# Kernel optimization log

Hardware: AMD Instinct MI355X
Metric: run time of the kernel (lower is better)

Reference implementation:

```python
import jax, jax.numpy as jnp
import numpy as np

B, S, H, NH = 4, 2048, 1024, 16
HD = H // NH


def setup_inputs() -> dict:
    key = jax.random.key(0)
    ks = jax.random.split(key, 9)
    s = 1.0 / np.sqrt(H)
    return {
        "x": jax.random.normal(ks[0], (B, S, H), dtype=jnp.float32),
        "wq": jax.random.normal(ks[1], (H, H), dtype=jnp.float32) * s,
        "bq": jax.random.normal(ks[2], (H,), dtype=jnp.float32) * 0.02,
        "wk": jax.random.normal(ks[3], (H, H), dtype=jnp.float32) * s,
        "bk": jax.random.normal(ks[4], (H,), dtype=jnp.float32) * 0.02,
        "wv": jax.random.normal(ks[5], (H, H), dtype=jnp.float32) * s,
        "bv": jax.random.normal(ks[6], (H,), dtype=jnp.float32) * 0.02,
        "wo": jax.random.normal(ks[7], (H, H), dtype=jnp.float32) * s,
        "bo": jax.random.normal(ks[8], (H,), dtype=jnp.float32) * 0.02,
    }


def reference(x, wq, bq, wk, bk, wv, bv, wo, bo):
    b, s, h = x.shape
    def heads(t):  # (b,s,h) -> (b,nh,s,hd)
        return t.reshape(b, s, NH, HD).transpose(0, 2, 1, 3)
    q = heads(x @ wq.T + bq)
    k = heads(x @ wk.T + bk)
    v = heads(x @ wv.T + bv)
    scores = jnp.einsum("bnqd,bnkd->bnqk", q, k) / np.sqrt(HD).astype(np.float32)
    causal = jnp.tril(jnp.ones((s, s), dtype=bool))
    scores = jnp.where(causal[None, None], scores, -jnp.inf)
    probs = jax.nn.softmax(scores, axis=-1)
    out = jnp.einsum("bnqk,bnkd->bnqd", probs, v)
    out = out.transpose(0, 2, 1, 3).reshape(b, s, h)
    return out @ wo.T + bo
```

## Files before the change

### kernel.cpp

```cpp
#include <hip/hip_runtime.h>
#include <hip/hip_bf16.h>

using bf16 = __bf16;
typedef __attribute__((ext_vector_type(4))) bf16 bf16x4;
typedef __attribute__((ext_vector_type(8))) bf16 bf16x8;
typedef __attribute__((ext_vector_type(4))) float f32x4;
typedef __attribute__((ext_vector_type(16))) float f32x16;

constexpr int kB = 4, kS = 2048, kH = 1024, kNH = 16, kHD = 64;
constexpr int kM = kB * kS;

__device__ __forceinline__ float exp2a(float x) {
  float r;
  asm("v_exp_f32 %0, %1" : "=v"(r) : "v"(x));
  return r;
}
__device__ __forceinline__ unsigned cvtpk(float a, float b) {
  unsigned r;
  asm("v_cvt_pk_bf16_f32 %0, %1, %2" : "=v"(r) : "v"(a), "v"(b));
  return r;
}
__device__ __forceinline__ void glds16(const bf16* g, bf16* l) {
  __builtin_amdgcn_global_load_lds(
      (const __attribute__((address_space(1))) unsigned*)g,
      (__attribute__((address_space(3))) unsigned*)l, 16, 0, 0);
}

__global__ __launch_bounds__(256) void cvt_all_kernel(
    const float* __restrict__ x, const float* __restrict__ w0,
    const float* __restrict__ w1, const float* __restrict__ w2,
    const float* __restrict__ w3, bf16* __restrict__ xb,
    bf16* __restrict__ wb) {
  const int blk = blockIdx.x;
  const float* src;
  bf16* dst;
  int rel;
  if (blk < kM) {
    src = x; dst = xb; rel = blk;
  } else {
    const int wi = (blk - kM) >> 10;
    rel = (blk - kM) & 1023;
    src = wi == 0 ? w0 : wi == 1 ? w1 : wi == 2 ? w2 : w3;
    dst = wb + (size_t)wi * kH * kH;
  }
  const size_t i = (size_t)rel * 256 + threadIdx.x;
  const float4 f = ((const float4*)src)[i];
  bf16x4 o;
  o[0] = (bf16)f.x; o[1] = (bf16)f.y; o[2] = (bf16)f.z; o[3] = (bf16)f.w;
  ((bf16x4*)dst)[i] = o;
}

template <int MODE>
__device__ __forceinline__ void mm_body(const bf16* __restrict__ A,
                                        const bf16* __restrict__ W,
                                        const float* __restrict__ bias,
                                        void* __restrict__ Cp, float scale) {
  __shared__ __align__(16) bf16 As[128 * 32];
  __shared__ __align__(16) bf16 Bs[128 * 32];
  const int tid = threadIdx.x;
  const int lane = tid & 63;
  const int wid = tid >> 6;
  const int wr = wid >> 1, wc = wid & 1;
  const int fr = lane & 15, fg = lane >> 4;
  const int bm = blockIdx.x * 128, bn = blockIdx.y * 128;
  const bf16* Ab = A + (size_t)bm * kH;
  const bf16* Wb = W + (size_t)bn * kH;
  const int srow = lane >> 2;
  const int scol = (lane & 3) * 8;
  const int rb0 = wid * 32, rb1 = wid * 32 + 16;

  f32x4 acc[4][4] = {};

  for (int k0 = 0; k0 < kH; k0 += 32) {
    __syncthreads();
    glds16(Ab + (size_t)(rb0 + srow) * kH + k0 + scol, As + rb0 * 32);
    glds16(Ab + (size_t)(rb1 + srow) * kH + k0 + scol, As + rb1 * 32);
    glds16(Wb + (size_t)(rb0 + srow) * kH + k0 + scol, Bs + rb0 * 32);
    glds16(Wb + (size_t)(rb1 + srow) * kH + k0 + scol, Bs + rb1 * 32);
    __syncthreads();

    bf16x8 af[4], bfv[4];
#pragma unroll
    for (int m = 0; m < 4; ++m)
      af[m] = *(const bf16x8*)(As + (wr * 64 + m * 16 + fr) * 32 + fg * 8);
#pragma unroll
    for (int n = 0; n < 4; ++n)
      bfv[n] = *(const bf16x8*)(Bs + (wc * 64 + n * 16 + fr) * 32 + fg * 8);
#pragma unroll
    for (int m = 0; m < 4; ++m)
#pragma unroll
      for (int n = 0; n < 4; ++n)
        acc[m][n] = __builtin_amdgcn_mfma_f32_16x16x32_bf16(af[m], bfv[n],
                                                            acc[m][n], 0, 0, 0);
  }

#pragma unroll
  for (int n = 0; n < 4; ++n) {
    const int nabs = bn + wc * 64 + n * 16 + fr;
    const float bv = bias[nabs];
#pragma unroll
    for (int m = 0; m < 4; ++m) {
      if (MODE == 2) {
        const int tok0 = bm + wr * 64 + m * 16 + fg * 4;
        const int b = tok0 >> 11, s0 = tok0 & (kS - 1);
        const int h = nabs >> 6, d = nabs & 63;
        bf16x4 pv;
#pragma unroll
        for (int reg = 0; reg < 4; ++reg) pv[reg] = (bf16)(acc[m][n][reg] + bv);
        *(bf16x4*)((bf16*)Cp + (((size_t)(b * kNH + h) * kHD + d) * kS + s0)) = pv;
      } else {
#pragma unroll
        for (int reg = 0; reg < 4; ++reg) {
          const int tok = bm + wr * 64 + m * 16 + fg * 4 + reg;
          const float v = (acc[m][n][reg] + bv) * scale;
          if (MODE == 0) {
            ((float*)Cp)[(size_t)tok * kH + nabs] = v;
          } else {
            const int b = tok >> 11, s = tok & (kS - 1);
            const int h = nabs >> 6, d = nabs & 63;
            ((bf16*)Cp)[(((size_t)(b * kNH + h)) * kS + s) * kHD + d] = (bf16)v;
          }
        }
      }
    }
  }
}

__global__ __launch_bounds__(256) void qkv_kernel(
    const bf16* __restrict__ xb, const bf16* __restrict__ wb,
    const float* __restrict__ bq, const float* __restrict__ bk,
    const float* __restrict__ bv, bf16* __restrict__ qh,
    bf16* __restrict__ kh, bf16* __restrict__ vh) {
  const int z = blockIdx.z;
  const bf16* W = wb + (size_t)z * kH * kH;
  if (z == 0) mm_body<1>(xb, W, bq, qh, 0.125f * 1.44269504f);
  else if (z == 1) mm_body<1>(xb, W, bk, kh, 1.f);
  else mm_body<2>(xb, W, bv, vh, 1.f);
}

__global__ __launch_bounds__(256) void oproj_kernel(
    const bf16* __restrict__ ab, const bf16* __restrict__ wob,
    const float* __restrict__ bo, float* __restrict__ out) {
  mm_body<0>(ab, wob, bo, out, 1.f);
}

__global__ __launch_bounds__(256) void attn_kernel(
    const bf16* __restrict__ Qh, const bf16* __restrict__ Kh,
    const bf16* __restrict__ Vt, bf16* __restrict__ Ab) {
  __shared__ __align__(16) bf16 Ks[64 * 64];
  __shared__ __align__(16) bf16 Vs[64 * 64];
  const int tid = threadIdx.x;
  const int lane = tid & 63;
  const int wid = tid >> 6;
  const int l31 = lane & 31;
  const int hi = lane >> 5;
  const int bh = blockIdx.x;
  const int qt = gridDim.y - 1 - blockIdx.y;
  const int b = bh >> 4, h = bh & (kNH - 1);

  const int qfirst = qt * 128 + wid * 32;
  const int qrow = qfirst + l31;

  const bf16* Qg = Qh + (size_t)bh * kS * kHD;
  const bf16* Kg = Kh + (size_t)bh * kS * kHD;
  const bf16* Vg = Vt + (size_t)bh * kHD * kS;

  bf16x8 qf[4];
#pragma unroll
  for (int kb = 0; kb < 4; ++kb)
    qf[kb] = *(const bf16x8*)(Qg + (size_t)qrow * kHD + kb * 16 + hi * 8);

  f32x16 Oa0 = {}, Oa1 = {};
  float lreg = 0.f;

  const int sr = tid >> 2;
  const int sc = tid & 3;
  const int nt64 = qt * 2 + 2;

  for (int kt = 0; kt < nt64; ++kt) {
    const int kt0 = kt * 64;
    const bf16x8 kr0 = *(const bf16x8*)(Kg + (size_t)(kt0 + sr) * kHD + sc * 8);
    const bf16x8 kr1 = *(const bf16x8*)(Kg + (size_t)(kt0 + sr) * kHD + (sc + 4) * 8);
    const bf16x8 vr0 = *(const bf16x8*)(Vg + (size_t)sr * kS + kt0 + sc * 8);
    const bf16x8 vr1 = *(const bf16x8*)(Vg + (size_t)sr * kS + kt0 + (sc + 4) * 8);
    __syncthreads();
    *(bf16x8*)((char*)Ks + sr * 128 + ((sc ^ (sr & 7)) << 4)) = kr0;
    *(bf16x8*)((char*)Ks + sr * 128 + (((sc + 4) ^ (sr & 7)) << 4)) = kr1;
    *(bf16x8*)((char*)Vs + sr * 128 + ((sc ^ (sr & 7)) << 4)) = vr0;
    *(bf16x8*)((char*)Vs + sr * 128 + (((sc + 4) ^ (sr & 7)) << 4)) = vr1;
    __syncthreads();

#pragma unroll
    for (int st = 0; st < 2; ++st) {
      const int kabs = kt0 + st * 32;
      if (kabs > qfirst) continue;
      const bool diag = (kabs == qfirst);

      f32x16 S = {};
      {
        const int row = st * 32 + l31;
        const char* krow = (const char*)Ks + row * 128;
#pragma unroll
        for (int kb = 0; kb < 4; ++kb) {
          const int slot = (kb * 2 + hi) ^ (row & 7);
          const bf16x8 kf = *(const bf16x8*)(krow + slot * 16);
          S = __builtin_amdgcn_mfma_f32_32x32x16_bf16(kf, qf[kb], S, 0, 0, 0);
        }
      }
      bf16x8 vf0[2], vf1[2];
#pragma unroll
      for (int kb2 = 0; kb2 < 2; ++kb2) {
        const int d0 = l31, d1 = 32 + l31;
        const int c = st * 4 + kb2 * 2 + hi;
        vf0[kb2] = *(const bf16x8*)((char*)Vs + d0 * 128 + ((c ^ (d0 & 7)) << 4));
        vf1[kb2] = *(const bf16x8*)((char*)Vs + d1 * 128 + ((c ^ (d1 & 7)) << 4));
      }

      float p[16];
      float ps = 0.f;
      if (diag) {
#pragma unroll
        for (int r = 0; r < 16; ++r) {
          const int key = kabs + (r & 3) + 8 * (r >> 2) + 4 * hi;
          float s2 = S[r] - 8.f;
          if (key > qrow) s2 = -3.0e38f;
          p[r] = exp2a(s2);
          ps += p[r];
        }
      } else {
#pragma unroll
        for (int r = 0; r < 16; ++r) {
          p[r] = exp2a(S[r] - 8.f);
          ps += p[r];
        }
      }
      ps += __shfl_xor(ps, 32, 64);
      lreg += ps;

      bf16x8 pf[2];
#pragma unroll
      for (int kb2 = 0; kb2 < 2; ++kb2) {
        const int o = kb2 * 8;
        unsigned a01 = cvtpk(p[o + 0], p[o + 1]);
        unsigned a45 = cvtpk(p[o + 4], p[o + 5]);
        asm("v_permlane32_swap_b32 %0, %1" : "+v"(a01), "+v"(a45));
        unsigned a23 = cvtpk(p[o + 2], p[o + 3]);
        unsigned a67 = cvtpk(p[o + 6], p[o + 7]);
        asm("v_permlane32_swap_b32 %0, %1" : "+v"(a23), "+v"(a67));
        union { unsigned u[4]; bf16x8 v; } t;
        t.u[0] = a01; t.u[1] = a23; t.u[2] = a45; t.u[3] = a67;
        pf[kb2] = t.v;
      }

#pragma unroll
      for (int kb2 = 0; kb2 < 2; ++kb2) {
        Oa0 = __builtin_amdgcn_mfma_f32_32x32x16_bf16(vf0[kb2], pf[kb2], Oa0, 0, 0, 0);
        Oa1 = __builtin_amdgcn_mfma_f32_32x32x16_bf16(vf1[kb2], pf[kb2], Oa1, 0, 0, 0);
      }
    }
  }

  const float rl = 1.f / lreg;
  bf16* const orow = Ab + ((size_t)b * kS + qrow) * kH + h * 64;
#pragma unroll
  for (int rq = 0; rq < 4; ++rq) {
    bf16x4 o0, o1;
#pragma unroll
    for (int j = 0; j < 4; ++j) {
      o0[j] = (bf16)(Oa0[rq * 4 + j] * rl);
      o1[j] = (bf16)(Oa1[rq * 4 + j] * rl);
    }
    *(bf16x4*)(orow + rq * 8 + hi * 4) = o0;
    *(bf16x4*)(orow + 32 + rq * 8 + hi * 4) = o1;
  }
}

extern "C" void kernel_launch(void* const* d_in, const int* in_sizes, int n_in,
                              void* d_out, int out_size, void* d_ws,
                              size_t ws_size, hipStream_t stream) {
  const float* x = (const float*)d_in[0];
  const float* wq = (const float*)d_in[1];
  const float* bq = (const float*)d_in[2];
  const float* wk = (const float*)d_in[3];
  const float* bk = (const float*)d_in[4];
  const float* wv = (const float*)d_in[5];
  const float* bv = (const float*)d_in[6];
  const float* wo = (const float*)d_in[7];
  const float* bo = (const float*)d_in[8];
  float* out = (float*)d_out;

  const size_t perHead = (size_t)kB * kNH * kS * kHD;
  bf16* xb = (bf16*)d_ws;
  bf16* wb = xb + (size_t)kM * kH;
  bf16* qh = wb + (size_t)4 * kH * kH;
  bf16* kh = qh + perHead;
  bf16* vh = kh + perHead;
  bf16* ab = vh + perHead;

  dim3 blk(256);
  cvt_all_kernel<<<dim3(kM + 4 * 1024), blk, 0, stream>>>(x, wq, wk, wv, wo,
                                                          xb, wb);
  qkv_kernel<<<dim3(kM / 128, kH / 128, 3), blk, 0, stream>>>(
      xb, wb, bq, bk, bv, qh, kh, vh);
  attn_kernel<<<dim3(kB * kNH, kS / 128), blk, 0, stream>>>(qh, kh, vh, ab);
  oproj_kernel<<<dim3(kM / 128, kH / 128), blk, 0, stream>>>(
      ab, wb + (size_t)3 * kH * kH, bo, out);
}
```

Measured before the change: 163.9 us.

## Rewrite QKV GEMM as 256x128 double-buffered 8-wave kernel with XCD remap

Replaces the templated QKV GEMM with a dedicated 512-thread kernel using 256x128 tiles and K=64 steps. It double-buffers LDS through direct global-to-LDS loads with XOR swizzle, interleaves MFMA phases with barriers and priority hints, and remaps block IDs across XCDs for L2 locality. The aim is to hide global load latency and raise data reuse in the dominant GEMM. The attention softmax also drops the constant -8 offset in the exponent, which risks overflow if scores grow large.

```diff
diff --git a/kernel.cpp b/kernel.cpp
--- a/kernel.cpp
+++ b/kernel.cpp
@@ -50,11 +50,133 @@
   ((bf16x4*)dst)[i] = o;
 }
 
-template <int MODE>
-__device__ __forceinline__ void mm_body(const bf16* __restrict__ A,
-                                        const bf16* __restrict__ W,
-                                        const float* __restrict__ bias,
-                                        void* __restrict__ Cp, float scale) {
+constexpr int kNT = 16;
+
+__global__ __launch_bounds__(512) void qkv8_kernel(
+    const bf16* __restrict__ xb, const bf16* __restrict__ wb,
+    const float* __restrict__ bq, const float* __restrict__ bk,
+    const float* __restrict__ bv, bf16* __restrict__ qh,
+    bf16* __restrict__ kh, bf16* __restrict__ vh) {
+  __shared__ __align__(16) bf16 As[2][256 * 64];
+  __shared__ __align__(16) bf16 Bs[2][128 * 64];
+  const int tid = threadIdx.x;
+  const int lane = tid & 63;
+  const int wid = tid >> 6;
+  const int wr = wid & 3;
+  const int wc = wid >> 2;
+  const int fr = lane & 15, fg = lane >> 4;
+
+  const int orig = blockIdx.x;
+  const int wg = (orig & 7) * 96 + (orig >> 3);
+  const int mb = wg & 31;
+  const int nb = wg >> 5;
+  const int bn_g = nb * 128;
+  const int z = bn_g >> 10;
+  const int bn = bn_g & 1023;
+
+  const bf16* Ab = xb + (size_t)mb * 256 * kH;
+  const bf16* Wb = wb + (size_t)z * kH * kH + (size_t)bn * kH;
+
+  const int s_r = lane >> 3;
+  const int s_cs = ((lane & 7) ^ (lane >> 3)) * 8;
+
+  f32x4 acc[4][4] = {};
+  bf16x8 bfr[4];
+
+#define ST(buf, kt)                                                          \
+  do {                                                                       \
+    const int k0_ = (kt) * 64;                                               \
+    _Pragma("unroll") for (int i = 0; i < 4; ++i) {                          \
+      const int rb = wid * 32 + i * 8;                                       \
+      glds16(Ab + (size_t)(rb + s_r) * kH + k0_ + s_cs, As[buf] + rb * 64);  \
+    }                                                                        \
+    _Pragma("unroll") for (int i = 0; i < 2; ++i) {                          \
+      const int rb = wid * 16 + i * 8;                                       \
+      glds16(Wb + (size_t)(rb + s_r) * kH + k0_ + s_cs, Bs[buf] + rb * 64);  \
+    }                                                                        \
+  } while (0)
+
+#define PH(buf, mlo, k2, DOB)                                                \
+  do {                                                                       \
+    const int swzA0 = (((k2)*4 + fg) ^ (fr & 7)) * 8;                        \
+    bf16x8 a0 = *(const bf16x8*)(As[buf] +                                   \
+        (wr * 64 + (mlo)*16 + fr) * 64 + swzA0);                             \
+    bf16x8 a1 = *(const bf16x8*)(As[buf] +                                   \
+        (wr * 64 + ((mlo)+1)*16 + fr) * 64 + swzA0);                         \
+    if (DOB) {                                                               \
+      _Pragma("unroll") for (int n = 0; n < 4; ++n)                          \
+        bfr[n] = *(const bf16x8*)(Bs[buf] +                                  \
+            (wc * 64 + n * 16 + fr) * 64 + swzA0);                           \
+    }                                                                        \
+    __builtin_amdgcn_s_barrier();                                            \
+    asm volatile("s_waitcnt lgkmcnt(0)" ::: "memory");                       \
+    __builtin_amdgcn_sched_barrier(0);                                       \
+    __builtin_amdgcn_s_setprio(1);                                           \
+    _Pragma("unroll") for (int n = 0; n < 4; ++n) {                          \
+      acc[(mlo)][n] = __builtin_amdgcn_mfma_f32_16x16x32_bf16(               \
+          a0, bfr[n], acc[(mlo)][n], 0, 0, 0);                               \
+      acc[(mlo)+1][n] = __builtin_amdgcn_mfma_f32_16x16x32_bf16(             \
+          a1, bfr[n], acc[(mlo)+1][n], 0, 0, 0);                             \
+    }                                                                        \
+    __builtin_amdgcn_s_setprio(0);                                           \
+    __builtin_amdgcn_s_barrier();                                            \
+  } while (0)
+
+  ST(0, 0);
+  ST(1, 1);
+  for (int t = 0; t < kNT; ++t) {
+    if (t < kNT - 1) {
+      asm volatile("s_waitcnt vmcnt(6)" ::: "memory");
+    } else {
+      asm volatile("s_waitcnt vmcnt(0)" ::: "memory");
+    }
+    __builtin_amdgcn_sched_barrier(0);
+    __builtin_amdgcn_s_barrier();
+    if ((t & 1) == 0) {
+      PH(0, 0, 0, 1); PH(0, 2, 0, 0); PH(0, 0, 1, 1); PH(0, 2, 1, 0);
+      if (t + 2 < kNT) ST(0, t + 2);
+    } else {
+      PH(1, 0, 0, 1); PH(1, 2, 0, 0); PH(1, 0, 1, 1); PH(1, 2, 1, 0);
+      if (t + 2 < kNT) ST(1, t + 2);
+    }
+  }
+#undef ST
+#undef PH
+
+  const float* bias = z == 0 ? bq : z == 1 ? bk : bv;
+  const float scale = z == 0 ? 0.125f * 1.44269504f : 1.f;
+#pragma unroll
+  for (int n = 0; n < 4; ++n) {
+    const int nabs = bn + wc * 64 + n * 16 + fr;
+    const float bv_ = bias[nabs];
+#pragma unroll
+    for (int m = 0; m < 4; ++m) {
+      if (z == 2) {
+        const int tok0 = mb * 256 + wr * 64 + m * 16 + fg * 4;
+        const int bb = tok0 >> 11, s0 = tok0 & (kS - 1);
+        const int hh = nabs >> 6, d = nabs & 63;
+        bf16x4 pv;
+#pragma unroll
+        for (int reg = 0; reg < 4; ++reg) pv[reg] = (bf16)(acc[m][n][reg] + bv_);
+        *(bf16x4*)(vh + (((size_t)(bb * kNH + hh) * kHD + d) * kS + s0)) = pv;
+      } else {
+        bf16* out = z == 0 ? qh : kh;
+#pragma unroll
+        for (int reg = 0; reg < 4; ++reg) {
+          const int tok = mb * 256 + wr * 64 + m * 16 + fg * 4 + reg;
+          const float v = (acc[m][n][reg] + bv_) * scale;
+          const int bb = tok >> 11, s = tok & (kS - 1);
+          const int hh = nabs >> 6, d = nabs & 63;
+          out[(((size_t)(bb * kNH + hh)) * kS + s) * kHD + d] = (bf16)v;
+        }
+      }
+    }
+  }
+}
+
+__global__ __launch_bounds__(256) void oproj_kernel(
+    const bf16* __restrict__ A, const bf16* __restrict__ W,
+    const float* __restrict__ bias, float* __restrict__ Cp) {
   __shared__ __align__(16) bf16 As[128 * 32];
   __shared__ __align__(16) bf16 Bs[128 * 32];
   const int tid = threadIdx.x;
@@ -99,49 +221,13 @@
     const int nabs = bn + wc * 64 + n * 16 + fr;
     const float bv = bias[nabs];
 #pragma unroll
-    for (int m = 0; m < 4; ++m) {
-      if (MODE == 2) {
-        const int tok0 = bm + wr * 64 + m * 16 + fg * 4;
-        const int b = tok0 >> 11, s0 = tok0 & (kS - 1);
-        const int h = nabs >> 6, d = nabs & 63;
-        bf16x4 pv;
-#pragma unroll
-        for (int reg = 0; reg < 4; ++reg) pv[reg] = (bf16)(acc[m][n][reg] + bv);
-        *(bf16x4*)((bf16*)Cp + (((size_t)(b * kNH + h) * kHD + d) * kS + s0)) = pv;
-      } else {
-#pragma unroll
-        for (int reg = 0; reg < 4; ++reg) {
-          const int tok = bm + wr * 64 + m * 16 + fg * 4 + reg;
-          const float v = (acc[m][n][reg] + bv) * scale;
-          if (MODE == 0) {
-            ((float*)Cp)[(size_t)tok * kH + nabs] = v;
-          } else {
-            const int b = tok >> 11, s = tok & (kS - 1);
-            const int h = nabs >> 6, d = nabs & 63;
-            ((bf16*)Cp)[(((size_t)(b * kNH + h)) * kS + s) * kHD + d] = (bf16)v;
-          }
-        }
-      }
-    }
-  }
-}
-
-__global__ __launch_bounds__(256) void qkv_kernel(
-    const bf16* __restrict__ xb, const bf16* __restrict__ wb,
-    const float* __restrict__ bq, const float* __restrict__ bk,
-    const float* __restrict__ bv, bf16* __restrict__ qh,
-    bf16* __restrict__ kh, bf16* __restrict__ vh) {
-  const int z = blockIdx.z;
-  const bf16* W = wb + (size_t)z * kH * kH;
-  if (z == 0) mm_body<1>(xb, W, bq, qh, 0.125f * 1.44269504f);
-  else if (z == 1) mm_body<1>(xb, W, bk, kh, 1.f);
-  else mm_body<2>(xb, W, bv, vh, 1.f);
-}
-
-__global__ __launch_bounds__(256) void oproj_kernel(
-    const bf16* __restrict__ ab, const bf16* __restrict__ wob,
-    const float* __restrict__ bo, float* __restrict__ out) {
-  mm_body<0>(ab, wob, bo, out, 1.f);
+    for (int m = 0; m < 4; ++m)
+#pragma unroll
+      for (int reg = 0; reg < 4; ++reg) {
+        const int tok = bm + wr * 64 + m * 16 + fg * 4 + reg;
+        Cp[(size_t)tok * kH + nabs] = acc[m][n][reg] + bv;
+      }
+  }
 }
 
 __global__ __launch_bounds__(256) void attn_kernel(
@@ -222,7 +308,7 @@
 #pragma unroll
         for (int r = 0; r < 16; ++r) {
           const int key = kabs + (r & 3) + 8 * (r >> 2) + 4 * hi;
-          float s2 = S[r] - 8.f;
+          float s2 = S[r];
           if (key > qrow) s2 = -3.0e38f;
           p[r] = exp2a(s2);
           ps += p[r];
@@ -230,7 +316,7 @@
       } else {
 #pragma unroll
         for (int r = 0; r < 16; ++r) {
-          p[r] = exp2a(S[r] - 8.f);
+          p[r] = exp2a(S[r]);
           ps += p[r];
         }
       }
@@ -297,12 +383,12 @@
   bf16* vh = kh + perHead;
   bf16* ab = vh + perHead;
 
-  dim3 blk(256);
-  cvt_all_kernel<<<dim3(kM + 4 * 1024), blk, 0, stream>>>(x, wq, wk, wv, wo,
-                                                          xb, wb);
-  qkv_kernel<<<dim3(kM / 128, kH / 128, 3), blk, 0, stream>>>(
-      xb, wb, bq, bk, bv, qh, kh, vh);
-  attn_kernel<<<dim3(kB * kNH, kS / 128), blk, 0, stream>>>(qh, kh, vh, ab);
-  oproj_kernel<<<dim3(kM / 128, kH / 128), blk, 0, stream>>>(
+  cvt_all_kernel<<<dim3(kM + 4 * 1024), dim3(256), 0, stream>>>(
+      x, wq, wk, wv, wo, xb, wb);
+  qkv8_kernel<<<dim3(768), dim3(512), 0, stream>>>(xb, wb, bq, bk, bv, qh, kh,
+                                                   vh);
+  attn_kernel<<<dim3(kB * kNH, kS / 128), dim3(256), 0, stream>>>(qh, kh, vh,
+                                                                  ab);
+  oproj_kernel<<<dim3(kM / 128, kH / 128), dim3(256), 0, stream>>>(
       ab, wb + (size_t)3 * kH * kH, bo, out);
 }
```

Result: slower. 182.0 us (+11.1%).
